# Optimization experiments

Measured on AMD Instinct MI355X. Metric: run time of the kernel, lower is better.

The kernel has to match this reference:

```python
import jax, jax.numpy as jnp
import numpy as np

WINDOW_SIZES = (1, 2, 3)
COV_DIM = 128
MEM_DIM = 128
BATCH = 8192


def setup_inputs() -> dict:
    rng = np.random.default_rng(0)
    sizes = rng.integers(16, 64, size=BATCH)
    total = int(sizes.sum())  # ~327k tokens
    key = jax.random.key(0)
    ks = jax.random.split(key, 10)
    s = 0.05
    inp = {
        "x": jax.random.normal(ks[0], (total, COV_DIM), jnp.float32),
        "sizes": jnp.asarray(sizes, jnp.int32),
    }
    for i, w in enumerate(WINDOW_SIZES):
        inp[f"conv_w{i}"] = jax.random.normal(ks[1 + 2 * i], (MEM_DIM, COV_DIM, w), jnp.float32) * s
        inp[f"conv_b{i}"] = jax.random.normal(ks[2 + 2 * i], (MEM_DIM,), jnp.float32) * s
    inp["lin_w"] = jax.random.normal(ks[7], (MEM_DIM, len(WINDOW_SIZES) * MEM_DIM), jnp.float32) * s
    inp["lin_b"] = jax.random.normal(ks[8], (MEM_DIM,), jnp.float32) * s
    return inp


def _temporal_conv(x, w, b):
    # x: [T, C], w: [M, C, k] -> [T-k+1, M]  (valid 1D conv, as nn.Conv1d)
    y = jax.lax.conv_general_dilated(
        x.T[None],  # [1, C, T]
        w,
        window_strides=(1,),
        padding="VALID",
        dimension_numbers=("NCH", "OIH", "NCH"),
    )[0]  # [M, L]
    return y.T + b


def _dmax(h, sizes, window_size, batch):
    # Ragged per-segment max over dim 0 of the concatenated conv output.
    # Segment i covers rows [off_i, off_i + sizes[i] - window_size + 1) where
    # off_i is the exclusive cumsum of sizes (DMax advances start_idx by sizes[i]).
    L = h.shape[0]  # total - window_size + 1
    cum = jnp.cumsum(sizes)  # [B], inclusive
    p = jnp.arange(L)
    seg = jnp.searchsorted(cum, p, side="right")  # segment owning row p
    valid = p + (window_size - 1) < cum[seg]  # within sizes[i]-w+1 prefix
    seg = jnp.where(valid, seg, batch)  # dump invalid rows in a trash segment
    return jax.ops.segment_max(h, seg, num_segments=batch + 1)[:batch]


def reference(x, sizes, conv_w0, conv_b0, conv_w1, conv_b1, conv_w2, conv_b2, lin_w, lin_b):
    batch = sizes.shape[0]
    convs = ((conv_w0, conv_b0), (conv_w1, conv_b1), (conv_w2, conv_b2))
    pools = []
    for wsz, (cw, cb) in zip(WINDOW_SIZES, convs):
        h = jax.nn.relu(_temporal_conv(x, cw, cb))  # [T-w+1, M]
        pools.append(_dmax(h, sizes, wsz, batch))  # [B, M]
    concat = jnp.concatenate(pools, axis=1)  # [B, 3M]
    return jnp.tanh(concat @ lin_w.T + lin_b)  # [B, M]
```

## Files before the change

kernel.cpp:

```cpp
#include <hip/hip_runtime.h>
#include <hip/hip_bf16.h>

typedef __bf16 bf16x8 __attribute__((ext_vector_type(8)));
typedef float  f32x4  __attribute__((ext_vector_type(4)));

#define MFMA16(a, b, c) __builtin_amdgcn_mfma_f32_16x16x32_bf16((a), (b), (c), 0, 0, 0)

__global__ void k_scan(const int* __restrict__ sizes, int* __restrict__ offsets) {
  __shared__ int part[256];
  const int t = threadIdx.x;
  const int base = t * 32;
  int v[32];
  int s = 0;
#pragma unroll
  for (int i = 0; i < 32; ++i) { v[i] = sizes[base + i]; s += v[i]; }
  part[t] = s;
  __syncthreads();
  for (int d = 1; d < 256; d <<= 1) {
    int add = (t >= d) ? part[t - d] : 0;
    __syncthreads();
    part[t] += add;
    __syncthreads();
  }
  int run = (t == 0) ? 0 : part[t - 1];
#pragma unroll
  for (int i = 0; i < 32; ++i) { offsets[base + i] = run; run += v[i]; }
}

__global__ void k_pack(const float* __restrict__ w0, const float* __restrict__ w1,
                       const float* __restrict__ w2, const float* __restrict__ lw,
                       __bf16* __restrict__ Wpack,
                       __bf16* __restrict__ Lhi, __bf16* __restrict__ Llo) {
  const int bid = blockIdx.x, t = threadIdx.x;
  if (bid < 48) {
    const int nt = bid, sl = nt >> 3, f = nt & 7;
    const int kt = t >> 6, lane = t & 63;
    const float* src; int kw, jj;
    if      (sl == 0) { src = w0; kw = 1; jj = 0; }
    else if (sl == 1) { src = w1; kw = 2; jj = 0; }
    else if (sl == 2) { src = w1; kw = 2; jj = 1; }
    else if (sl == 3) { src = w2; kw = 3; jj = 0; }
    else if (sl == 4) { src = w2; kw = 3; jj = 1; }
    else              { src = w2; kw = 3; jj = 2; }
    const int feat  = f * 16 + (lane & 15);
    const int cbase = kt * 32 + ((lane >> 4) << 3);
    __bf16* dst = Wpack + ((((nt * 4 + kt) << 6) + lane) << 3);
#pragma unroll
    for (int j = 0; j < 8; ++j)
      dst[j] = (__bf16)src[(feat * 128 + cbase + j) * kw + jj];
  } else {
    const int idx = (bid - 48) * 256 + t;
    const int j = idx & 7, lane = (idx >> 3) & 63, rest = idx >> 9;
    const int kt = rest % 12, nt = rest / 12;
    const int o = nt * 16 + (lane & 15);
    const int q = kt * 32 + ((lane >> 4) << 3) + j;
    const float v = lw[o * 384 + q];
    const __bf16 hi = (__bf16)v;
    Lhi[idx] = hi;
    Llo[idx] = (__bf16)(v - (float)hi);
  }
}

__global__ __launch_bounds__(256, 3)
void k_conv(const float* __restrict__ x, const int* __restrict__ sizes,
            const int* __restrict__ offsets,
            const float* __restrict__ cb0, const float* __restrict__ cb1,
            const float* __restrict__ cb2,
            const bf16x8* __restrict__ Wpack,
            __bf16* __restrict__ Phi, __bf16* __restrict__ Plo) {
  __shared__ __bf16 xh[64 * 136];
  __shared__ __bf16 xl[64 * 136];
  const int b = blockIdx.x;
  const int s = sizes[b];
  const long off = offsets[b];
  const int t = threadIdx.x;
  const int MT = (s + 15) >> 4;

  const int quads = s << 5;
  for (int qi = t; qi < quads; qi += 256) {
    const int e = qi << 2, r = e >> 7, c = e & 127;
    const float4 v = *(const float4*)(x + (off + r) * 128 + c);
    __bf16* dh = &xh[r * 136 + c];
    __bf16* dl = &xl[r * 136 + c];
    dh[0] = (__bf16)v.x; dl[0] = (__bf16)(v.x - (float)dh[0]);
    dh[1] = (__bf16)v.y; dl[1] = (__bf16)(v.y - (float)dh[1]);
    dh[2] = (__bf16)v.z; dl[2] = (__bf16)(v.z - (float)dh[2]);
    dh[3] = (__bf16)v.w; dl[3] = (__bf16)(v.w - (float)dh[3]);
  }
  const int padquads = ((MT << 4) - s) << 5;
  for (int qi = t; qi < padquads; qi += 256) {
    const int e = (qi << 2) + (s << 7), r = e >> 7, c = e & 127;
    __bf16* dh = &xh[r * 136 + c];
    __bf16* dl = &xl[r * 136 + c];
#pragma unroll
    for (int j = 0; j < 4; ++j) { dh[j] = (__bf16)0.f; dl[j] = (__bf16)0.f; }
  }
  __syncthreads();

  const int wid = t >> 6, lane = t & 63;
  const int lo16 = lane & 15, g = lane >> 4;

#pragma unroll
  for (int fi = 0; fi < 2; ++fi) {
    const int ft = wid + (fi << 2);
    const int feat = ft * 16 + lo16;
#pragma unroll
    for (int pass = 0; pass < 2; ++pass) {
      f32x4 acc[4][3];
#pragma unroll
      for (int mt = 0; mt < 4; ++mt)
#pragma unroll
        for (int sl = 0; sl < 3; ++sl)
          acc[mt][sl] = f32x4{0.f, 0.f, 0.f, 0.f};

#pragma unroll
      for (int kt = 0; kt < 4; ++kt) {
        bf16x8 bf[3];
#pragma unroll
        for (int sl = 0; sl < 3; ++sl) {
          const int slg = pass * 3 + sl;
          bf[sl] = Wpack[(((slg * 8 + ft) * 4 + kt) << 6) + lane];
        }
#pragma unroll
        for (int mt = 0; mt < 4; ++mt) {
          if (mt < MT) {
            const int aoff = (mt * 16 + lo16) * 136 + kt * 32 + (g << 3);
            const bf16x8 ah = *(const bf16x8*)&xh[aoff];
            const bf16x8 al = *(const bf16x8*)&xl[aoff];
            acc[mt][0] = MFMA16(ah, bf[0], acc[mt][0]);
            acc[mt][1] = MFMA16(ah, bf[1], acc[mt][1]);
            acc[mt][2] = MFMA16(ah, bf[2], acc[mt][2]);
            acc[mt][0] = MFMA16(al, bf[0], acc[mt][0]);
            acc[mt][1] = MFMA16(al, bf[1], acc[mt][1]);
            acc[mt][2] = MFMA16(al, bf[2], acc[mt][2]);
          }
        }
      }

      if (pass == 0) {
        float m1 = -1e30f, m2 = -1e30f;
#pragma unroll
        for (int mt = 0; mt < 4; ++mt) {
          if (mt >= MT) continue;
#pragma unroll
          for (int v = 0; v < 4; ++v) {
            float s2v;
            if (v < 3) {
              s2v = acc[mt][2][v + 1];
            } else {
              const float up = __shfl(acc[mt][2][0], lane + 16);
              const float dn = __shfl(acc[(mt < 3) ? mt + 1 : mt][2][0], lo16);
              s2v = (g < 3) ? up : dn;
            }
            const int lrow = mt * 16 + g * 4 + v;
            if (lrow < s)     m1 = fmaxf(m1, acc[mt][0][v]);
            if (lrow < s - 1) m2 = fmaxf(m2, acc[mt][1][v] + s2v);
          }
        }
        m1 = fmaxf(m1, __shfl_xor(m1, 16)); m1 = fmaxf(m1, __shfl_xor(m1, 32));
        m2 = fmaxf(m2, __shfl_xor(m2, 16)); m2 = fmaxf(m2, __shfl_xor(m2, 32));
        if (g == 0) {
          const float p1 = fmaxf(m1 + cb0[feat], 0.f);
          const float p2 = fmaxf(m2 + cb1[feat], 0.f);
          const __bf16 h1 = (__bf16)p1, h2 = (__bf16)p2;
          Phi[(long)b * 384 + feat]       = h1;
          Plo[(long)b * 384 + feat]       = (__bf16)(p1 - (float)h1);
          Phi[(long)b * 384 + 128 + feat] = h2;
          Plo[(long)b * 384 + 128 + feat] = (__bf16)(p2 - (float)h2);
        }
      } else {
        float m3 = -1e30f;
#pragma unroll
        for (int mt = 0; mt < 4; ++mt) {
          if (mt >= MT) continue;
#pragma unroll
          for (int v = 0; v < 4; ++v) {
            float s4v, s5v;
            if (v < 3) {
              s4v = acc[mt][1][v + 1];
            } else {
              const float up = __shfl(acc[mt][1][0], lane + 16);
              const float dn = __shfl(acc[(mt < 3) ? mt + 1 : mt][1][0], lo16);
              s4v = (g < 3) ? up : dn;
            }
            if (v < 2) {
              s5v = acc[mt][2][v + 2];
            } else {
              const float up = __shfl(acc[mt][2][v - 2], lane + 16);
              const float dn = __shfl(acc[(mt < 3) ? mt + 1 : mt][2][v - 2], lo16);
              s5v = (g < 3) ? up : dn;
            }
            const int lrow = mt * 16 + g * 4 + v;
            if (lrow < s - 2) m3 = fmaxf(m3, acc[mt][0][v] + s4v + s5v);
          }
        }
        m3 = fmaxf(m3, __shfl_xor(m3, 16)); m3 = fmaxf(m3, __shfl_xor(m3, 32));
        if (g == 0) {
          const float p3 = fmaxf(m3 + cb2[feat], 0.f);
          const __bf16 h3 = (__bf16)p3;
          Phi[(long)b * 384 + 256 + feat] = h3;
          Plo[(long)b * 384 + 256 + feat] = (__bf16)(p3 - (float)h3);
        }
      }
    }
  }
}

__global__ __launch_bounds__(256, 2)
void k_lin(const __bf16* __restrict__ Phi, const __bf16* __restrict__ Plo,
           const bf16x8* __restrict__ Lhi, const bf16x8* __restrict__ Llo,
           const float* __restrict__ lb, float* __restrict__ out) {
  __shared__ __bf16 ph[32 * 392];
  __shared__ __bf16 pl[32 * 392];
  const int blk = blockIdx.x, t = threadIdx.x;
  const long rbase = (long)blk * 32;
#pragma unroll
  for (int i = 0; i < 6; ++i) {
    const int ci = t + (i << 8);
    const int r = ci / 48, cc = ci % 48;
    *(int4*)&ph[r * 392 + (cc << 3)] = *(const int4*)&Phi[(rbase + r) * 384 + (cc << 3)];
    *(int4*)&pl[r * 392 + (cc << 3)] = *(const int4*)&Plo[(rbase + r) * 384 + (cc << 3)];
  }
  __syncthreads();
  const int wid = t >> 6, lane = t & 63;
  const int lo16 = lane & 15, g = lane >> 4;
#pragma unroll
  for (int ni = 0; ni < 2; ++ni) {
    const int nt = wid + (ni << 2);
    f32x4 acc[2];
    acc[0] = f32x4{0.f, 0.f, 0.f, 0.f};
    acc[1] = f32x4{0.f, 0.f, 0.f, 0.f};
#pragma unroll
    for (int kt = 0; kt < 12; ++kt) {
      const bf16x8 bh = Lhi[((nt * 12 + kt) << 6) + lane];
      const bf16x8 bl = Llo[((nt * 12 + kt) << 6) + lane];
#pragma unroll
      for (int mt = 0; mt < 2; ++mt) {
        const int aoff = (mt * 16 + lo16) * 392 + kt * 32 + (g << 3);
        const bf16x8 ah = *(const bf16x8*)&ph[aoff];
        const bf16x8 al = *(const bf16x8*)&pl[aoff];
        acc[mt] = MFMA16(ah, bh, acc[mt]);
        acc[mt] = MFMA16(al, bh, acc[mt]);
        acc[mt] = MFMA16(ah, bl, acc[mt]);
      }
    }
    const int o = nt * 16 + lo16;
    const float bias = lb[o];
#pragma unroll
    for (int mt = 0; mt < 2; ++mt)
#pragma unroll
      for (int v = 0; v < 4; ++v) {
        const int r = mt * 16 + g * 4 + v;
        const float val = acc[mt][v] + bias;
        out[(rbase + r) * 128 + o] = 1.f - 2.f / (__expf(2.f * val) + 1.f);
      }
  }
}

extern "C" void kernel_launch(void* const* d_in, const int* in_sizes, int n_in,
                              void* d_out, int out_size, void* d_ws, size_t ws_size,
                              hipStream_t stream) {
  const float* x   = (const float*)d_in[0];
  const int* sizes = (const int*)d_in[1];
  const float* w0  = (const float*)d_in[2];
  const float* cb0 = (const float*)d_in[3];
  const float* w1  = (const float*)d_in[4];
  const float* cb1 = (const float*)d_in[5];
  const float* w2  = (const float*)d_in[6];
  const float* cb2 = (const float*)d_in[7];
  const float* lw  = (const float*)d_in[8];
  const float* lb  = (const float*)d_in[9];

  char* ws = (char*)d_ws;
  size_t o = 0;
  int*    offsets = (int*)ws;                 o += 32768;
  __bf16* Wpack   = (__bf16*)(ws + o);        o += 196608;
  __bf16* Lhi     = (__bf16*)(ws + o);        o += 98304;
  __bf16* Llo     = (__bf16*)(ws + o);        o += 98304;
  __bf16* Phi     = (__bf16*)(ws + o);        o += 8192L * 384 * 2;
  __bf16* Plo     = (__bf16*)(ws + o);        o += 8192L * 384 * 2;

  k_scan<<<1, 256, 0, stream>>>(sizes, offsets);
  k_pack<<<240, 256, 0, stream>>>(w0, w1, w2, lw, Wpack, Lhi, Llo);
  k_conv<<<8192, 256, 0, stream>>>(x, sizes, offsets, cb0, cb1, cb2,
                                   (const bf16x8*)Wpack, Phi, Plo);
  k_lin<<<256, 256, 0, stream>>>(Phi, Plo, (const bf16x8*)Lhi,
                                 (const bf16x8*)Llo, lb, (float*)d_out);
}
```

Measured before the change: 365.8 us.

## Drop x low-part split, fuse conv passes, merge prep kernels, shrink linear tiles

Result: faster. 340.9 us (-6.8%).

```diff
diff --git a/kernel.cpp b/kernel.cpp
--- a/kernel.cpp
+++ b/kernel.cpp
@@ -2,37 +2,36 @@
 #include <hip/hip_bf16.h>
 
 typedef __bf16 bf16x8 __attribute__((ext_vector_type(8)));
+typedef __bf16 bf16x4 __attribute__((ext_vector_type(4)));
 typedef float  f32x4  __attribute__((ext_vector_type(4)));
 
 #define MFMA16(a, b, c) __builtin_amdgcn_mfma_f32_16x16x32_bf16((a), (b), (c), 0, 0, 0)
 
-__global__ void k_scan(const int* __restrict__ sizes, int* __restrict__ offsets) {
-  __shared__ int part[256];
-  const int t = threadIdx.x;
-  const int base = t * 32;
-  int v[32];
-  int s = 0;
-#pragma unroll
-  for (int i = 0; i < 32; ++i) { v[i] = sizes[base + i]; s += v[i]; }
-  part[t] = s;
-  __syncthreads();
-  for (int d = 1; d < 256; d <<= 1) {
-    int add = (t >= d) ? part[t - d] : 0;
-    __syncthreads();
-    part[t] += add;
-    __syncthreads();
-  }
-  int run = (t == 0) ? 0 : part[t - 1];
-#pragma unroll
-  for (int i = 0; i < 32; ++i) { offsets[base + i] = run; run += v[i]; }
-}
-
-__global__ void k_pack(const float* __restrict__ w0, const float* __restrict__ w1,
+__global__ void k_prep(const int* __restrict__ sizes, int* __restrict__ offsets,
+                       const float* __restrict__ w0, const float* __restrict__ w1,
                        const float* __restrict__ w2, const float* __restrict__ lw,
                        __bf16* __restrict__ Wpack,
                        __bf16* __restrict__ Lhi, __bf16* __restrict__ Llo) {
   const int bid = blockIdx.x, t = threadIdx.x;
-  if (bid < 48) {
+  if (bid == 240) {
+    __shared__ int part[256];
+    const int base = t * 32;
+    int v[32];
+    int s = 0;
+#pragma unroll
+    for (int i = 0; i < 32; ++i) { v[i] = sizes[base + i]; s += v[i]; }
+    part[t] = s;
+    __syncthreads();
+    for (int d = 1; d < 256; d <<= 1) {
+      int add = (t >= d) ? part[t - d] : 0;
+      __syncthreads();
+      part[t] += add;
+      __syncthreads();
+    }
+    int run = (t == 0) ? 0 : part[t - 1];
+#pragma unroll
+    for (int i = 0; i < 32; ++i) { offsets[base + i] = run; run += v[i]; }
+  } else if (bid < 48) {
     const int nt = bid, sl = nt >> 3, f = nt & 7;
     const int kt = t >> 6, lane = t & 63;
     const float* src; int kw, jj;
@@ -69,7 +68,6 @@
             const bf16x8* __restrict__ Wpack,
             __bf16* __restrict__ Phi, __bf16* __restrict__ Plo) {
   __shared__ __bf16 xh[64 * 136];
-  __shared__ __bf16 xl[64 * 136];
   const int b = blockIdx.x;
   const int s = sizes[b];
   const long off = offsets[b];
@@ -80,20 +78,14 @@
   for (int qi = t; qi < quads; qi += 256) {
     const int e = qi << 2, r = e >> 7, c = e & 127;
     const float4 v = *(const float4*)(x + (off + r) * 128 + c);
-    __bf16* dh = &xh[r * 136 + c];
-    __bf16* dl = &xl[r * 136 + c];
-    dh[0] = (__bf16)v.x; dl[0] = (__bf16)(v.x - (float)dh[0]);
-    dh[1] = (__bf16)v.y; dl[1] = (__bf16)(v.y - (float)dh[1]);
-    dh[2] = (__bf16)v.z; dl[2] = (__bf16)(v.z - (float)dh[2]);
-    dh[3] = (__bf16)v.w; dl[3] = (__bf16)(v.w - (float)dh[3]);
+    bf16x4 h; h[0] = (__bf16)v.x; h[1] = (__bf16)v.y;
+              h[2] = (__bf16)v.z; h[3] = (__bf16)v.w;
+    *(bf16x4*)&xh[r * 136 + c] = h;
   }
   const int padquads = ((MT << 4) - s) << 5;
   for (int qi = t; qi < padquads; qi += 256) {
     const int e = (qi << 2) + (s << 7), r = e >> 7, c = e & 127;
-    __bf16* dh = &xh[r * 136 + c];
-    __bf16* dl = &xl[r * 136 + c];
-#pragma unroll
-    for (int j = 0; j < 4; ++j) { dh[j] = (__bf16)0.f; dl[j] = (__bf16)0.f; }
+    *(bf16x4*)&xh[r * 136 + c] = bf16x4{(__bf16)0.f, (__bf16)0.f, (__bf16)0.f, (__bf16)0.f};
   }
   __syncthreads();
 
@@ -104,118 +96,95 @@
   for (int fi = 0; fi < 2; ++fi) {
     const int ft = wid + (fi << 2);
     const int feat = ft * 16 + lo16;
-#pragma unroll
-    for (int pass = 0; pass < 2; ++pass) {
-      f32x4 acc[4][3];
-#pragma unroll
-      for (int mt = 0; mt < 4; ++mt)
-#pragma unroll
-        for (int sl = 0; sl < 3; ++sl)
-          acc[mt][sl] = f32x4{0.f, 0.f, 0.f, 0.f};
-
-#pragma unroll
-      for (int kt = 0; kt < 4; ++kt) {
-        bf16x8 bf[3];
-#pragma unroll
-        for (int sl = 0; sl < 3; ++sl) {
-          const int slg = pass * 3 + sl;
-          bf[sl] = Wpack[(((slg * 8 + ft) * 4 + kt) << 6) + lane];
-        }
-#pragma unroll
-        for (int mt = 0; mt < 4; ++mt) {
-          if (mt < MT) {
-            const int aoff = (mt * 16 + lo16) * 136 + kt * 32 + (g << 3);
-            const bf16x8 ah = *(const bf16x8*)&xh[aoff];
-            const bf16x8 al = *(const bf16x8*)&xl[aoff];
-            acc[mt][0] = MFMA16(ah, bf[0], acc[mt][0]);
-            acc[mt][1] = MFMA16(ah, bf[1], acc[mt][1]);
-            acc[mt][2] = MFMA16(ah, bf[2], acc[mt][2]);
-            acc[mt][0] = MFMA16(al, bf[0], acc[mt][0]);
-            acc[mt][1] = MFMA16(al, bf[1], acc[mt][1]);
-            acc[mt][2] = MFMA16(al, bf[2], acc[mt][2]);
-          }
+    f32x4 acc[4][6];
+#pragma unroll
+    for (int mt = 0; mt < 4; ++mt)
+#pragma unroll
+      for (int sl = 0; sl < 6; ++sl)
+        acc[mt][sl] = f32x4{0.f, 0.f, 0.f, 0.f};
+
+#pragma unroll
+    for (int kt = 0; kt < 4; ++kt) {
+      bf16x8 bf[6];
+#pragma unroll
+      for (int sl = 0; sl < 6; ++sl)
+        bf[sl] = Wpack[(((sl * 8 + ft) * 4 + kt) << 6) + lane];
+#pragma unroll
+      for (int mt = 0; mt < 4; ++mt) {
+        if (mt < MT) {
+          const bf16x8 a =
+              *(const bf16x8*)&xh[(mt * 16 + lo16) * 136 + kt * 32 + (g << 3)];
+#pragma unroll
+          for (int sl = 0; sl < 6; ++sl)
+            acc[mt][sl] = MFMA16(a, bf[sl], acc[mt][sl]);
         }
       }
-
-      if (pass == 0) {
-        float m1 = -1e30f, m2 = -1e30f;
-#pragma unroll
-        for (int mt = 0; mt < 4; ++mt) {
-          if (mt >= MT) continue;
-#pragma unroll
-          for (int v = 0; v < 4; ++v) {
-            float s2v;
-            if (v < 3) {
-              s2v = acc[mt][2][v + 1];
-            } else {
-              const float up = __shfl(acc[mt][2][0], lane + 16);
-              const float dn = __shfl(acc[(mt < 3) ? mt + 1 : mt][2][0], lo16);
-              s2v = (g < 3) ? up : dn;
-            }
-            const int lrow = mt * 16 + g * 4 + v;
-            if (lrow < s)     m1 = fmaxf(m1, acc[mt][0][v]);
-            if (lrow < s - 1) m2 = fmaxf(m2, acc[mt][1][v] + s2v);
-          }
-        }
-        m1 = fmaxf(m1, __shfl_xor(m1, 16)); m1 = fmaxf(m1, __shfl_xor(m1, 32));
-        m2 = fmaxf(m2, __shfl_xor(m2, 16)); m2 = fmaxf(m2, __shfl_xor(m2, 32));
-        if (g == 0) {
-          const float p1 = fmaxf(m1 + cb0[feat], 0.f);
-          const float p2 = fmaxf(m2 + cb1[feat], 0.f);
-          const __bf16 h1 = (__bf16)p1, h2 = (__bf16)p2;
-          Phi[(long)b * 384 + feat]       = h1;
-          Plo[(long)b * 384 + feat]       = (__bf16)(p1 - (float)h1);
-          Phi[(long)b * 384 + 128 + feat] = h2;
-          Plo[(long)b * 384 + 128 + feat] = (__bf16)(p2 - (float)h2);
-        }
-      } else {
-        float m3 = -1e30f;
-#pragma unroll
-        for (int mt = 0; mt < 4; ++mt) {
-          if (mt >= MT) continue;
-#pragma unroll
-          for (int v = 0; v < 4; ++v) {
-            float s4v, s5v;
-            if (v < 3) {
-              s4v = acc[mt][1][v + 1];
-            } else {
-              const float up = __shfl(acc[mt][1][0], lane + 16);
-              const float dn = __shfl(acc[(mt < 3) ? mt + 1 : mt][1][0], lo16);
-              s4v = (g < 3) ? up : dn;
-            }
-            if (v < 2) {
-              s5v = acc[mt][2][v + 2];
-            } else {
-              const float up = __shfl(acc[mt][2][v - 2], lane + 16);
-              const float dn = __shfl(acc[(mt < 3) ? mt + 1 : mt][2][v - 2], lo16);
-              s5v = (g < 3) ? up : dn;
-            }
-            const int lrow = mt * 16 + g * 4 + v;
-            if (lrow < s - 2) m3 = fmaxf(m3, acc[mt][0][v] + s4v + s5v);
-          }
-        }
-        m3 = fmaxf(m3, __shfl_xor(m3, 16)); m3 = fmaxf(m3, __shfl_xor(m3, 32));
-        if (g == 0) {
-          const float p3 = fmaxf(m3 + cb2[feat], 0.f);
-          const __bf16 h3 = (__bf16)p3;
-          Phi[(long)b * 384 + 256 + feat] = h3;
-          Plo[(long)b * 384 + 256 + feat] = (__bf16)(p3 - (float)h3);
-        }
+    }
+
+    float m1 = -1e30f, m2 = -1e30f, m3 = -1e30f;
+#pragma unroll
+    for (int mt = 0; mt < 4; ++mt) {
+      if (mt >= MT) continue;
+#pragma unroll
+      for (int v = 0; v < 4; ++v) {
+        float s2v;
+        if (v < 3) {
+          s2v = acc[mt][2][v + 1];
+        } else {
+          const float up = __shfl(acc[mt][2][0], lane + 16);
+          const float dn = __shfl(acc[(mt < 3) ? mt + 1 : mt][2][0], lo16);
+          s2v = (g < 3) ? up : dn;
+        }
+        float s4v;
+        if (v < 3) {
+          s4v = acc[mt][4][v + 1];
+        } else {
+          const float up = __shfl(acc[mt][4][0], lane + 16);
+          const float dn = __shfl(acc[(mt < 3) ? mt + 1 : mt][4][0], lo16);
+          s4v = (g < 3) ? up : dn;
+        }
+        float s5v;
+        if (v < 2) {
+          s5v = acc[mt][5][v + 2];
+        } else {
+          const float up = __shfl(acc[mt][5][v - 2], lane + 16);
+          const float dn = __shfl(acc[(mt < 3) ? mt + 1 : mt][5][v - 2], lo16);
+          s5v = (g < 3) ? up : dn;
+        }
+        const int lrow = mt * 16 + g * 4 + v;
+        if (lrow < s)     m1 = fmaxf(m1, acc[mt][0][v]);
+        if (lrow < s - 1) m2 = fmaxf(m2, acc[mt][1][v] + s2v);
+        if (lrow < s - 2) m3 = fmaxf(m3, acc[mt][3][v] + s4v + s5v);
       }
     }
-  }
-}
-
-__global__ __launch_bounds__(256, 2)
+    m1 = fmaxf(m1, __shfl_xor(m1, 16)); m1 = fmaxf(m1, __shfl_xor(m1, 32));
+    m2 = fmaxf(m2, __shfl_xor(m2, 16)); m2 = fmaxf(m2, __shfl_xor(m2, 32));
+    m3 = fmaxf(m3, __shfl_xor(m3, 16)); m3 = fmaxf(m3, __shfl_xor(m3, 32));
+    if (g == 0) {
+      const float p1 = fmaxf(m1 + cb0[feat], 0.f);
+      const float p2 = fmaxf(m2 + cb1[feat], 0.f);
+      const float p3 = fmaxf(m3 + cb2[feat], 0.f);
+      const __bf16 h1 = (__bf16)p1, h2 = (__bf16)p2, h3 = (__bf16)p3;
+      Phi[(long)b * 384 + feat]       = h1;
+      Plo[(long)b * 384 + feat]       = (__bf16)(p1 - (float)h1);
+      Phi[(long)b * 384 + 128 + feat] = h2;
+      Plo[(long)b * 384 + 128 + feat] = (__bf16)(p2 - (float)h2);
+      Phi[(long)b * 384 + 256 + feat] = h3;
+      Plo[(long)b * 384 + 256 + feat] = (__bf16)(p3 - (float)h3);
+    }
+  }
+}
+
+__global__ __launch_bounds__(256, 4)
 void k_lin(const __bf16* __restrict__ Phi, const __bf16* __restrict__ Plo,
            const bf16x8* __restrict__ Lhi, const bf16x8* __restrict__ Llo,
            const float* __restrict__ lb, float* __restrict__ out) {
-  __shared__ __bf16 ph[32 * 392];
-  __shared__ __bf16 pl[32 * 392];
+  __shared__ __bf16 ph[16 * 392];
+  __shared__ __bf16 pl[16 * 392];
   const int blk = blockIdx.x, t = threadIdx.x;
-  const long rbase = (long)blk * 32;
-#pragma unroll
-  for (int i = 0; i < 6; ++i) {
+  const long rbase = (long)blk * 16;
+#pragma unroll
+  for (int i = 0; i < 3; ++i) {
     const int ci = t + (i << 8);
     const int r = ci / 48, cc = ci % 48;
     *(int4*)&ph[r * 392 + (cc << 3)] = *(const int4*)&Phi[(rbase + r) * 384 + (cc << 3)];
@@ -227,33 +196,26 @@
 #pragma unroll
   for (int ni = 0; ni < 2; ++ni) {
     const int nt = wid + (ni << 2);
-    f32x4 acc[2];
-    acc[0] = f32x4{0.f, 0.f, 0.f, 0.f};
-    acc[1] = f32x4{0.f, 0.f, 0.f, 0.f};
+    f32x4 acc = f32x4{0.f, 0.f, 0.f, 0.f};
 #pragma unroll
     for (int kt = 0; kt < 12; ++kt) {
       const bf16x8 bh = Lhi[((nt * 12 + kt) << 6) + lane];
       const bf16x8 bl = Llo[((nt * 12 + kt) << 6) + lane];
-#pragma unroll
-      for (int mt = 0; mt < 2; ++mt) {
-        const int aoff = (mt * 16 + lo16) * 392 + kt * 32 + (g << 3);
-        const bf16x8 ah = *(const bf16x8*)&ph[aoff];
-        const bf16x8 al = *(const bf16x8*)&pl[aoff];
-        acc[mt] = MFMA16(ah, bh, acc[mt]);
-        acc[mt] = MFMA16(al, bh, acc[mt]);
-        acc[mt] = MFMA16(ah, bl, acc[mt]);
-      }
+      const int aoff = lo16 * 392 + kt * 32 + (g << 3);
+      const bf16x8 ah = *(const bf16x8*)&ph[aoff];
+      const bf16x8 al = *(const bf16x8*)&pl[aoff];
+      acc = MFMA16(ah, bh, acc);
+      acc = MFMA16(al, bh, acc);
+      acc = MFMA16(ah, bl, acc);
     }
     const int o = nt * 16 + lo16;
     const float bias = lb[o];
 #pragma unroll
-    for (int mt = 0; mt < 2; ++mt)
-#pragma unroll
-      for (int v = 0; v < 4; ++v) {
-        const int r = mt * 16 + g * 4 + v;
-        const float val = acc[mt][v] + bias;
-        out[(rbase + r) * 128 + o] = 1.f - 2.f / (__expf(2.f * val) + 1.f);
-      }
+    for (int v = 0; v < 4; ++v) {
+      const int r = g * 4 + v;
+      const float val = acc[v] + bias;
+      out[(rbase + r) * 128 + o] = 1.f - 2.f / (__expf(2.f * val) + 1.f);
+    }
   }
 }
 
@@ -280,10 +242,9 @@
   __bf16* Phi     = (__bf16*)(ws + o);        o += 8192L * 384 * 2;
   __bf16* Plo     = (__bf16*)(ws + o);        o += 8192L * 384 * 2;
 
-  k_scan<<<1, 256, 0, stream>>>(sizes, offsets);
-  k_pack<<<240, 256, 0, stream>>>(w0, w1, w2, lw, Wpack, Lhi, Llo);
+  k_prep<<<241, 256, 0, stream>>>(sizes, offsets, w0, w1, w2, lw, Wpack, Lhi, Llo);
   k_conv<<<8192, 256, 0, stream>>>(x, sizes, offsets, cb0, cb1, cb2,
                                    (const bf16x8*)Wpack, Phi, Plo);
-  k_lin<<<256, 256, 0, stream>>>(Phi, Plo, (const bf16x8*)Lhi,
+  k_lin<<<512, 256, 0, stream>>>(Phi, Plo, (const bf16x8*)Lhi,
                                  (const bf16x8*)Llo, lb, (float*)d_out);
 }
```
